# Performance work log

Measured on AMD Instinct MI355X. Metric: run time of the kernel, lower is better.

## Reference

```python
import jax, jax.numpy as jnp
import numpy as np

SEQ = 4096
INPUT_DIM = 64
D_MODEL = 1024
LAYERS = 2


def setup_inputs() -> dict:
    key = jax.random.key(0)
    ks = jax.random.split(key, 7)
    s = 1.0 / np.sqrt(D_MODEL)  # torch-style uniform-ish scale, keeps gates unsaturated
    return {
        "input_market_values": jax.random.normal(ks[0], (SEQ, INPUT_DIM), jnp.float32),
        "W1": jax.random.normal(ks[1], (D_MODEL, INPUT_DIM), jnp.float32) / np.sqrt(INPUT_DIM),
        "b1": jax.random.normal(ks[2], (D_MODEL,), jnp.float32) * s,
        "Wih": jax.random.normal(ks[3], (LAYERS, 4 * D_MODEL, D_MODEL), jnp.float32) * s,
        "Whh": jax.random.normal(ks[4], (LAYERS, 4 * D_MODEL, D_MODEL), jnp.float32) * s,
        "bih": jax.random.normal(ks[5], (LAYERS, 4 * D_MODEL), jnp.float32) * s,
        "bhh": jax.random.normal(ks[6], (LAYERS, 4 * D_MODEL), jnp.float32) * s,
    }


def _lstm_layer(x, Wih, Whh, bih, bhh):
    # x: (T, H_in). PyTorch LSTM gate order: i, f, g, o.
    H = Whh.shape[1]
    b = bih + bhh
    xg = x @ Wih.T + b  # precompute input contribution for all timesteps: (T, 4H)

    def step(carry, xgt):
        h, c = carry
        g = xgt + h @ Whh.T
        i, f, gg, o = jnp.split(g, 4, axis=-1)
        c = jax.nn.sigmoid(f) * c + jax.nn.sigmoid(i) * jnp.tanh(gg)
        h = jax.nn.sigmoid(o) * jnp.tanh(c)
        return (h, c), h

    init = (jnp.zeros((H,), x.dtype), jnp.zeros((H,), x.dtype))
    _, hs = jax.lax.scan(step, init, xg)
    return hs  # (T, H)


def reference(input_market_values, W1, b1, Wih, Whh, bih, bhh):
    # Per-step Linear + LeakyReLU (equivalent to applying it to the whole sequence)
    x = jax.nn.leaky_relu(input_market_values @ W1.T + b1)  # (T, D)
    for l in range(Wih.shape[0]):  # small fixed number of layers
        x = _lstm_layer(x, Wih[l], Whh[l], bih[l], bhh[l])
    # Original returns leaky_relu of the top-layer output at the final timestep, shape (1,1,D)
    return jax.nn.leaky_relu(x[-1]).reshape(1, 1, -1)
```

## Files before the change

### kernel.cpp

```cpp
#include <hip/hip_runtime.h>
#include <hip/hip_fp16.h>
#include <math.h>

#define T_SEQ 4096
#define DIN   64
#define DM    1024
#define G4    4096
#define LSTRIDE_W ((size_t)G4 * DM)
#define LSTRIDE_B ((size_t)G4)

#define SENT 0x7FC0DEADu

#define S_RING  32
#define S_RETRY 4
#define S_HIST  8

typedef unsigned long long u64;
typedef unsigned int u32;

#define PAUSE(n) do { __builtin_amdgcn_s_sleep(n); asm volatile("" ::: "memory"); } while (0)

__device__ __forceinline__ float sigmoidf_(float x) {
    return 1.0f / (1.0f + __expf(-x));
}
__device__ __forceinline__ float tanhf_(float x) {
    float ax = fabsf(x);
    float e  = __expf(-2.0f * ax);
    float t  = (1.0f - e) / (1.0f + e);
    return copysignf(t, x);
}
__device__ __forceinline__ float lrelu_(float x) {
    return x > 0.0f ? x : 0.01f * x;
}

__device__ __forceinline__ u32 pk2_(float x, float y) {
    typedef __fp16 hv2 __attribute__((ext_vector_type(2)));
    union { hv2 h; u32 u; } c;
    c.h = __builtin_amdgcn_cvt_pkrtz(x, y);
    return c.u;
}
#if __has_builtin(__builtin_amdgcn_fdot2)
__device__ __forceinline__ float d2a_(u32 a, u32 b, float acc) {
    typedef __fp16 hv2 __attribute__((ext_vector_type(2)));
    union { u32 u; hv2 h; } ua, ub;
    ua.u = a; ub.u = b;
    return __builtin_amdgcn_fdot2(ua.h, ub.h, acc, false);
}
#else
__device__ __forceinline__ float d2a_(u32 a, u32 b, float acc) {
    union { u32 u; __half2 h; } ua, ub;
    ua.u = a; ub.u = b;
    float2 fa = __half22float2(ua.h);
    float2 fb = __half22float2(ub.h);
    return acc + fa.x * fb.x + fa.y * fb.y;
}
#endif
__device__ __forceinline__ float dot8a_(uint4 q, uint4 h, float acc) {
    acc = d2a_(q.x, h.x, acc);
    acc = d2a_(q.y, h.y, acc);
    acc = d2a_(q.z, h.z, acc);
    acc = d2a_(q.w, h.w, acc);
    return acc;
}

__global__ __launch_bounds__(256) void k_input(const float* __restrict__ inp,
                                               const float* __restrict__ W1,
                                               const float* __restrict__ b1,
                                               float* __restrict__ x) {
    __shared__ float s_in[DIN];
    const int t   = blockIdx.x;
    const int tid = threadIdx.x;
    if (tid < DIN) s_in[tid] = inp[(size_t)t * DIN + tid];
    __syncthreads();
#pragma unroll
    for (int q = 0; q < 4; q++) {
        const int d = tid + q * 256;
        const float4* wr = (const float4*)(W1 + (size_t)d * DIN);
        float acc = 0.0f;
#pragma unroll
        for (int e = 0; e < 16; e++) {
            float4 w = wr[e];
            acc += w.x * s_in[e * 4 + 0] + w.y * s_in[e * 4 + 1] +
                   w.z * s_in[e * 4 + 2] + w.w * s_in[e * 4 + 3];
        }
        acc += b1[d];
        x[(size_t)t * DM + d] = lrelu_(acc);
    }
}

__global__ __launch_bounds__(256) void k_gemm(const float* __restrict__ A,
                                              const float* __restrict__ B,
                                              const float* __restrict__ bih,
                                              const float* __restrict__ bhh,
                                              float* __restrict__ C) {
    const int K = DM;
    __shared__ float As[16][132];
    __shared__ float Bs[16][132];
    const int tid = threadIdx.x;
    const int m0 = blockIdx.y * 128, n0 = blockIdx.x * 128;
    const int tx = tid & 15, ty = tid >> 4;
    const int lr = tid >> 1;
    const int lc = (tid & 1) * 8;

    float acc[8][8] = {};
    const float4* ag = (const float4*)(A + (size_t)(m0 + lr) * K + lc);
    const float4* bg = (const float4*)(B + (size_t)(n0 + lr) * K + lc);

    for (int k0 = 0; k0 < K; k0 += 16) {
        float4 a0 = ag[0], a1 = ag[1];
        float4 b0 = bg[0], b1v = bg[1];
        ag += 4; bg += 4;
        __syncthreads();
        As[lc + 0][lr] = a0.x; As[lc + 1][lr] = a0.y; As[lc + 2][lr] = a0.z; As[lc + 3][lr] = a0.w;
        As[lc + 4][lr] = a1.x; As[lc + 5][lr] = a1.y; As[lc + 6][lr] = a1.z; As[lc + 7][lr] = a1.w;
        Bs[lc + 0][lr] = b0.x; Bs[lc + 1][lr] = b0.y; Bs[lc + 2][lr] = b0.z; Bs[lc + 3][lr] = b0.w;
        Bs[lc + 4][lr] = b1v.x; Bs[lc + 5][lr] = b1v.y; Bs[lc + 6][lr] = b1v.z; Bs[lc + 7][lr] = b1v.w;
        __syncthreads();
#pragma unroll
        for (int k = 0; k < 16; k++) {
            float a[8], b[8];
            *(float4*)&a[0] = *(const float4*)&As[k][ty * 8 + 0];
            *(float4*)&a[4] = *(const float4*)&As[k][ty * 8 + 4];
            *(float4*)&b[0] = *(const float4*)&Bs[k][tx * 8 + 0];
            *(float4*)&b[4] = *(const float4*)&Bs[k][tx * 8 + 4];
#pragma unroll
            for (int i = 0; i < 8; i++)
#pragma unroll
                for (int j = 0; j < 8; j++)
                    acc[i][j] += a[i] * b[j];
        }
    }
    float bj[8];
#pragma unroll
    for (int j = 0; j < 8; j++) {
        int n = n0 + tx * 8 + j;
        bj[j] = bih[n] + bhh[n];
    }
#pragma unroll
    for (int i = 0; i < 8; i++) {
        float4 v0, v1;
        v0.x = acc[i][0] + bj[0]; v0.y = acc[i][1] + bj[1];
        v0.z = acc[i][2] + bj[2]; v0.w = acc[i][3] + bj[3];
        v1.x = acc[i][4] + bj[4]; v1.y = acc[i][5] + bj[5];
        v1.z = acc[i][6] + bj[6]; v1.w = acc[i][7] + bj[7];
        float* cp = C + (size_t)(m0 + ty * 8 + i) * G4 + n0 + tx * 8;
        *(float4*)(cp + 0) = v0;
        *(float4*)(cp + 4) = v1;
    }
}

__global__ __launch_bounds__(256) void k_clear(u32* __restrict__ p) {
    uint4 v; v.x = SENT; v.y = SENT; v.z = SENT; v.w = SENT;
    ((uint4*)p)[(size_t)blockIdx.x * 256 + threadIdx.x] = v;
}

__global__ __launch_bounds__(256, 2) void k_scan2(
        const float* __restrict__ xg,
        const float* __restrict__ Wih1,
        const float* __restrict__ Whh0,
        const float* __restrict__ Whh1,
        const float* __restrict__ bih1,
        const float* __restrict__ bhh1,
        u32* h0hist,
        u64* sl1,
        float* __restrict__ out) {
    const int tid  = threadIdx.x;
    const bool isL0 = (blockIdx.x < 256);
    const int w    = isL0 ? blockIdx.x : (blockIdx.x - 256);
    const int wv   = tid >> 6;
    const int ln   = tid & 63;
    const int rs   = tid >> 4;
    const int ck   = tid & 15;
    const int g_i  = rs & 3;
    const int r    = g_i * DM + w * 4 + wv;

    __shared__ uint4 hstA[2][16][9];
    __shared__ uint4 hstB[2][16][9];

    const int stc = tid >> 4;
    const int sto = tid & 15;

    if (isL0) {
        uint4 wr0[8];
        {
            const float4* gw = (const float4*)(Whh0 + (size_t)r * DM + ck * 64);
#pragma unroll
            for (int e = 0; e < 8; e++) {
                float4 a = gw[2 * e], b = gw[2 * e + 1];
                uint4 q;
                q.x = pk2_(a.x, a.y); q.y = pk2_(a.z, a.w);
                q.z = pk2_(b.x, b.y); q.w = pk2_(b.z, b.w);
                wr0[e] = q;
            }
        }
        float c0 = 0.f, h0v = 0.f;
        float xgv = (ck == 0) ? xg[r] : 0.f;

        for (int t = 0; t < T_SEQ; t++) {
            const int par = t & 1;
            if (t == 0) {
                ((u64*)&hstA[0][stc][0])[sto] = 0ull;
            } else {
                PAUSE(S_RING);
                const u32* hp = h0hist + (size_t)(t - 1) * DM + tid * 4;
                u32 v0, v1, v2, v3;
                for (;;) {
                    v0 = __hip_atomic_load(hp + 0, __ATOMIC_RELAXED, __HIP_MEMORY_SCOPE_AGENT);
                    v1 = __hip_atomic_load(hp + 1, __ATOMIC_RELAXED, __HIP_MEMORY_SCOPE_AGENT);
                    v2 = __hip_atomic_load(hp + 2, __ATOMIC_RELAXED, __HIP_MEMORY_SCOPE_AGENT);
                    v3 = __hip_atomic_load(hp + 3, __ATOMIC_RELAXED, __HIP_MEMORY_SCOPE_AGENT);
                    if ((v0 != SENT) & (v1 != SENT) & (v2 != SENT) & (v3 != SENT)) break;
                    PAUSE(S_RETRY);
                }
                u32 q0 = pk2_(__uint_as_float(v0), __uint_as_float(v1));
                u32 q1 = pk2_(__uint_as_float(v2), __uint_as_float(v3));
                ((u64*)&hstA[par][stc][0])[sto] = ((u64)q1 << 32) | q0;
            }
            __syncthreads();

            float acc = 0.f;
#pragma unroll
            for (int e = 0; e < 8; e++)
                acc = dot8a_(wr0[e], hstA[par][ck][e], acc);
#pragma unroll
            for (int m = 1; m <= 8; m <<= 1) acc += __shfl_xor(acc, m, 64);
            if (ck == 0) acc += xgv;

            float pi = __shfl(acc, 0, 64);
            float pf = __shfl(acc, 16, 64);
            float pg = __shfl(acc, 32, 64);
            float po = __shfl(acc, 48, 64);
            if (ln == 0) {
                c0 = sigmoidf_(pf) * c0 + sigmoidf_(pi) * tanhf_(pg);
                h0v = sigmoidf_(po) * tanhf_(c0);
                __hip_atomic_store(h0hist + (size_t)t * DM + w * 4 + wv,
                                   __float_as_uint(h0v),
                                   __ATOMIC_RELAXED, __HIP_MEMORY_SCOPE_AGENT);
            }
            float xgn = 0.f;
            if (ck == 0 && t + 1 < T_SEQ) xgn = xg[(size_t)(t + 1) * G4 + r];
            xgv = xgn;
        }
    } else {
        uint4 wi1[8], wh1[8];
        {
            const float4* ga = (const float4*)(Wih1 + (size_t)r * DM + ck * 64);
            const float4* gb = (const float4*)(Whh1 + (size_t)r * DM + ck * 64);
#pragma unroll
            for (int e = 0; e < 8; e++) {
                float4 a = ga[2 * e], b = ga[2 * e + 1];
                uint4 q;
                q.x = pk2_(a.x, a.y); q.y = pk2_(a.z, a.w);
                q.z = pk2_(b.x, b.y); q.w = pk2_(b.z, b.w);
                wi1[e] = q;
                a = gb[2 * e]; b = gb[2 * e + 1];
                q.x = pk2_(a.x, a.y); q.y = pk2_(a.z, a.w);
                q.z = pk2_(b.x, b.y); q.w = pk2_(b.z, b.w);
                wh1[e] = q;
            }
        }
        float b1s[4] = {0.f, 0.f, 0.f, 0.f};
        if (ln == 0) {
#pragma unroll
            for (int gg = 0; gg < 4; gg++)
                b1s[gg] = bih1[gg * DM + w * 4 + wv] + bhh1[gg * DM + w * 4 + wv];
        }
        float c1 = 0.f, h1v = 0.f;

        for (int t = 0; t < T_SEQ; t++) {
            const int par = t & 1;
            const u32* hp = h0hist + (size_t)t * DM + tid * 4;

            u32 v0 = __hip_atomic_load(hp + 0, __ATOMIC_RELAXED, __HIP_MEMORY_SCOPE_AGENT);
            u32 v1 = __hip_atomic_load(hp + 1, __ATOMIC_RELAXED, __HIP_MEMORY_SCOPE_AGENT);
            u32 v2 = __hip_atomic_load(hp + 2, __ATOMIC_RELAXED, __HIP_MEMORY_SCOPE_AGENT);
            u32 v3 = __hip_atomic_load(hp + 3, __ATOMIC_RELAXED, __HIP_MEMORY_SCOPE_AGENT);

            if (t > 0) PAUSE(S_RING);

            while ((v0 == SENT) | (v1 == SENT) | (v2 == SENT) | (v3 == SENT)) {
                PAUSE(S_HIST);
                v0 = __hip_atomic_load(hp + 0, __ATOMIC_RELAXED, __HIP_MEMORY_SCOPE_AGENT);
                v1 = __hip_atomic_load(hp + 1, __ATOMIC_RELAXED, __HIP_MEMORY_SCOPE_AGENT);
                v2 = __hip_atomic_load(hp + 2, __ATOMIC_RELAXED, __HIP_MEMORY_SCOPE_AGENT);
                v3 = __hip_atomic_load(hp + 3, __ATOMIC_RELAXED, __HIP_MEMORY_SCOPE_AGENT);
            }
            {
                u32 q0 = pk2_(__uint_as_float(v0), __uint_as_float(v1));
                u32 q1 = pk2_(__uint_as_float(v2), __uint_as_float(v3));
                ((u64*)&hstA[par][stc][0])[sto] = ((u64)q1 << 32) | q0;
            }

            if (t == 0) {
                ((u64*)&hstB[0][stc][0])[sto] = 0ull;
            } else {
                const u64* p1 = sl1 + (size_t)par * 1024 + tid * 4;
                const u32 want = (u32)t;
                u64 d0, d1, d2, d3;
                for (;;) {
                    d0 = __hip_atomic_load(p1 + 0, __ATOMIC_RELAXED, __HIP_MEMORY_SCOPE_AGENT);
                    d1 = __hip_atomic_load(p1 + 1, __ATOMIC_RELAXED, __HIP_MEMORY_SCOPE_AGENT);
                    d2 = __hip_atomic_load(p1 + 2, __ATOMIC_RELAXED, __HIP_MEMORY_SCOPE_AGENT);
                    d3 = __hip_atomic_load(p1 + 3, __ATOMIC_RELAXED, __HIP_MEMORY_SCOPE_AGENT);
                    bool ok = ((u32)(d0 >> 32) == want) & ((u32)(d1 >> 32) == want) &
                              ((u32)(d2 >> 32) == want) & ((u32)(d3 >> 32) == want);
                    if (ok) break;
                    PAUSE(S_RETRY);
                }
                u32 q0 = pk2_(__uint_as_float((u32)d0), __uint_as_float((u32)d1));
                u32 q1 = pk2_(__uint_as_float((u32)d2), __uint_as_float((u32)d3));
                ((u64*)&hstB[par][stc][0])[sto] = ((u64)q1 << 32) | q0;
            }
            __syncthreads();

            float a1 = 0.f, a2 = 0.f;
#pragma unroll
            for (int e = 0; e < 8; e++) {
                a1 = dot8a_(wi1[e], hstA[par][ck][e], a1);
                a2 = dot8a_(wh1[e], hstB[par][ck][e], a2);
            }
#pragma unroll
            for (int m = 1; m <= 8; m <<= 1) {
                a1 += __shfl_xor(a1, m, 64);
                a2 += __shfl_xor(a2, m, 64);
            }
            float pi = __shfl(a1, 0, 64)  + __shfl(a2, 0, 64);
            float pf = __shfl(a1, 16, 64) + __shfl(a2, 16, 64);
            float pg = __shfl(a1, 32, 64) + __shfl(a2, 32, 64);
            float po = __shfl(a1, 48, 64) + __shfl(a2, 48, 64);
            if (ln == 0) {
                pi += b1s[0]; pf += b1s[1]; pg += b1s[2]; po += b1s[3];
                c1 = sigmoidf_(pf) * c1 + sigmoidf_(pi) * tanhf_(pg);
                h1v = sigmoidf_(po) * tanhf_(c1);
                u64 v = ((u64)(u32)(t + 1) << 32) | (u64)__float_as_uint(h1v);
                __hip_atomic_store(sl1 + (size_t)((t + 1) & 1) * 1024 + w * 4 + wv,
                                   v, __ATOMIC_RELAXED, __HIP_MEMORY_SCOPE_AGENT);
            }
        }
        if (ln == 0) out[w * 4 + wv] = lrelu_(h1v);
    }
}

extern "C" void kernel_launch(void* const* d_in, const int* in_sizes, int n_in,
                              void* d_out, int out_size, void* d_ws, size_t ws_size,
                              hipStream_t stream) {
    const float* inp = (const float*)d_in[0];
    const float* W1  = (const float*)d_in[1];
    const float* b1  = (const float*)d_in[2];
    const float* Wih = (const float*)d_in[3];
    const float* Whh = (const float*)d_in[4];
    const float* bih = (const float*)d_in[5];
    const float* bhh = (const float*)d_in[6];
    float* out = (float*)d_out;

    float* x   = (float*)d_ws;
    float* xg  = x + (size_t)T_SEQ * DM;
    u64*   sl1 = (u64*)(xg + (size_t)T_SEQ * G4);
    u32*   h0hist = (u32*)x;
    (void)in_sizes; (void)n_in; (void)out_size; (void)ws_size;

    k_input<<<dim3(T_SEQ), dim3(256), 0, stream>>>(inp, W1, b1, x);

    k_gemm<<<dim3(32, 32), dim3(256), 0, stream>>>(x, Wih, bih, bhh, xg);

    k_clear<<<dim3(4096), dim3(256), 0, stream>>>(h0hist);

    k_scan2<<<dim3(512), dim3(256), 0, stream>>>(
        xg, Wih + LSTRIDE_W, Whh, Whh + LSTRIDE_W,
        bih + LSTRIDE_B, bhh + LSTRIDE_B, h0hist, sl1, out);
}
```

Before: 10.13 ms.

## Publish hidden states as fp16 history with sentinel polling and parallel gate activations

Both LSTM layers now publish each hidden value as a single fp16 halfword into per-timestep history buffers checked against a 16-bit sentinel. Consumers poll with one 64-bit atomic load per thread instead of four 32-bit loads, and the data goes straight to shared memory without repacking. Layer 1 uses a history buffer instead of the two-slot tagged ring and overlaps the input-side dot product with waiting for its own previous state. Gate nonlinearities are computed in parallel across lanes before the shuffle, and the sleep constants are retuned. The risk is that an fp16 result equal to the sentinel pattern (a NaN encoding) would make a consumer spin forever.

```diff
diff --git a/kernel.cpp b/kernel.cpp
--- a/kernel.cpp
+++ b/kernel.cpp
@@ -9,14 +9,16 @@
 #define LSTRIDE_W ((size_t)G4 * DM)
 #define LSTRIDE_B ((size_t)G4)
 
-#define SENT 0x7FC0DEADu
-
-#define S_RING  32
-#define S_RETRY 4
+#define SENT16 0xDEADu
+#define SENT32 0xDEADDEADu
+
+#define S_RING  40
+#define S_RETRY 6
 #define S_HIST  8
 
 typedef unsigned long long u64;
 typedef unsigned int u32;
+typedef unsigned short u16;
 
 #define PAUSE(n) do { __builtin_amdgcn_s_sleep(n); asm volatile("" ::: "memory"); } while (0)
 
@@ -61,6 +63,10 @@
     acc = d2a_(q.z, h.z, acc);
     acc = d2a_(q.w, h.w, acc);
     return acc;
+}
+__device__ __forceinline__ bool has_sent_(u64 v) {
+    return (((u32)v & 0xFFFFu) == SENT16) | ((((u32)v >> 16)) == SENT16) |
+           (((u32)(v >> 32) & 0xFFFFu) == SENT16) | (((u32)(v >> 48)) == SENT16);
 }
 
 __global__ __launch_bounds__(256) void k_input(const float* __restrict__ inp,
@@ -150,7 +156,7 @@
 }
 
 __global__ __launch_bounds__(256) void k_clear(u32* __restrict__ p) {
-    uint4 v; v.x = SENT; v.y = SENT; v.z = SENT; v.w = SENT;
+    uint4 v; v.x = SENT32; v.y = SENT32; v.z = SENT32; v.w = SENT32;
     ((uint4*)p)[(size_t)blockIdx.x * 256 + threadIdx.x] = v;
 }
 
@@ -161,8 +167,8 @@
         const float* __restrict__ Whh1,
         const float* __restrict__ bih1,
         const float* __restrict__ bhh1,
-        u32* h0hist,
-        u64* sl1,
+        u16* h0h,
+        u16* h1h,
         float* __restrict__ out) {
     const int tid  = threadIdx.x;
     const bool isL0 = (blockIdx.x < 256);
@@ -202,19 +208,14 @@
                 ((u64*)&hstA[0][stc][0])[sto] = 0ull;
             } else {
                 PAUSE(S_RING);
-                const u32* hp = h0hist + (size_t)(t - 1) * DM + tid * 4;
-                u32 v0, v1, v2, v3;
+                const u64* hp = (const u64*)(h0h + (size_t)(t - 1) * DM) + tid;
+                u64 v;
                 for (;;) {
-                    v0 = __hip_atomic_load(hp + 0, __ATOMIC_RELAXED, __HIP_MEMORY_SCOPE_AGENT);
-                    v1 = __hip_atomic_load(hp + 1, __ATOMIC_RELAXED, __HIP_MEMORY_SCOPE_AGENT);
-                    v2 = __hip_atomic_load(hp + 2, __ATOMIC_RELAXED, __HIP_MEMORY_SCOPE_AGENT);
-                    v3 = __hip_atomic_load(hp + 3, __ATOMIC_RELAXED, __HIP_MEMORY_SCOPE_AGENT);
-                    if ((v0 != SENT) & (v1 != SENT) & (v2 != SENT) & (v3 != SENT)) break;
+                    v = __hip_atomic_load(hp, __ATOMIC_RELAXED, __HIP_MEMORY_SCOPE_AGENT);
+                    if (!has_sent_(v)) break;
                     PAUSE(S_RETRY);
                 }
-                u32 q0 = pk2_(__uint_as_float(v0), __uint_as_float(v1));
-                u32 q1 = pk2_(__uint_as_float(v2), __uint_as_float(v3));
-                ((u64*)&hstA[par][stc][0])[sto] = ((u64)q1 << 32) | q0;
+                ((u64*)&hstA[par][stc][0])[sto] = v;
             }
             __syncthreads();
 
@@ -226,15 +227,16 @@
             for (int m = 1; m <= 8; m <<= 1) acc += __shfl_xor(acc, m, 64);
             if (ck == 0) acc += xgv;
 
-            float pi = __shfl(acc, 0, 64);
-            float pf = __shfl(acc, 16, 64);
-            float pg = __shfl(acc, 32, 64);
-            float po = __shfl(acc, 48, 64);
+            float act = ((ln >> 4) == 2) ? tanhf_(acc) : sigmoidf_(acc);
+            float ai = __shfl(act, 0, 64);
+            float af = __shfl(act, 16, 64);
+            float ag = __shfl(act, 32, 64);
+            float ao = __shfl(act, 48, 64);
             if (ln == 0) {
-                c0 = sigmoidf_(pf) * c0 + sigmoidf_(pi) * tanhf_(pg);
-                h0v = sigmoidf_(po) * tanhf_(c0);
-                __hip_atomic_store(h0hist + (size_t)t * DM + w * 4 + wv,
-                                   __float_as_uint(h0v),
+                c0  = af * c0 + ai * ag;
+                h0v = ao * tanhf_(c0);
+                u32 q = pk2_(h0v, h0v);
+                __hip_atomic_store(h0h + (size_t)t * DM + w * 4 + wv, (u16)(q & 0xFFFFu),
                                    __ATOMIC_RELAXED, __HIP_MEMORY_SCOPE_AGENT);
             }
             float xgn = 0.f;
@@ -259,82 +261,70 @@
                 wh1[e] = q;
             }
         }
-        float b1s[4] = {0.f, 0.f, 0.f, 0.f};
-        if (ln == 0) {
-#pragma unroll
-            for (int gg = 0; gg < 4; gg++)
-                b1s[gg] = bih1[gg * DM + w * 4 + wv] + bhh1[gg * DM + w * 4 + wv];
+        float bsel = 0.f;
+        if ((ln & 15) == 0) {
+            const int gg = ln >> 4;
+            bsel = bih1[gg * DM + w * 4 + wv] + bhh1[gg * DM + w * 4 + wv];
         }
         float c1 = 0.f, h1v = 0.f;
 
         for (int t = 0; t < T_SEQ; t++) {
             const int par = t & 1;
-            const u32* hp = h0hist + (size_t)t * DM + tid * 4;
-
-            u32 v0 = __hip_atomic_load(hp + 0, __ATOMIC_RELAXED, __HIP_MEMORY_SCOPE_AGENT);
-            u32 v1 = __hip_atomic_load(hp + 1, __ATOMIC_RELAXED, __HIP_MEMORY_SCOPE_AGENT);
-            u32 v2 = __hip_atomic_load(hp + 2, __ATOMIC_RELAXED, __HIP_MEMORY_SCOPE_AGENT);
-            u32 v3 = __hip_atomic_load(hp + 3, __ATOMIC_RELAXED, __HIP_MEMORY_SCOPE_AGENT);
+            const u64* hp0 = (const u64*)(h0h + (size_t)t * DM) + tid;
+            const u64* hp1 = (const u64*)(h1h + (size_t)(t > 0 ? t - 1 : 0) * DM) + tid;
+
+            u64 v0 = __hip_atomic_load(hp0, __ATOMIC_RELAXED, __HIP_MEMORY_SCOPE_AGENT);
 
             if (t > 0) PAUSE(S_RING);
 
-            while ((v0 == SENT) | (v1 == SENT) | (v2 == SENT) | (v3 == SENT)) {
+            while (has_sent_(v0)) {
                 PAUSE(S_HIST);
-                v0 = __hip_atomic_load(hp + 0, __ATOMIC_RELAXED, __HIP_MEMORY_SCOPE_AGENT);
-                v1 = __hip_atomic_load(hp + 1, __ATOMIC_RELAXED, __HIP_MEMORY_SCOPE_AGENT);
-                v2 = __hip_atomic_load(hp + 2, __ATOMIC_RELAXED, __HIP_MEMORY_SCOPE_AGENT);
-                v3 = __hip_atomic_load(hp + 3, __ATOMIC_RELAXED, __HIP_MEMORY_SCOPE_AGENT);
-            }
-            {
-                u32 q0 = pk2_(__uint_as_float(v0), __uint_as_float(v1));
-                u32 q1 = pk2_(__uint_as_float(v2), __uint_as_float(v3));
-                ((u64*)&hstA[par][stc][0])[sto] = ((u64)q1 << 32) | q0;
-            }
+                v0 = __hip_atomic_load(hp0, __ATOMIC_RELAXED, __HIP_MEMORY_SCOPE_AGENT);
+            }
+            ((u64*)&hstA[par][stc][0])[sto] = v0;
+
+            u64 v1 = 0;
+            if (t > 0)
+                v1 = __hip_atomic_load(hp1, __ATOMIC_RELAXED, __HIP_MEMORY_SCOPE_AGENT);
+            __syncthreads();
+
+            float a1 = 0.f;
+#pragma unroll
+            for (int e = 0; e < 8; e++)
+                a1 = dot8a_(wi1[e], hstA[par][ck][e], a1);
+#pragma unroll
+            for (int m = 1; m <= 8; m <<= 1) a1 += __shfl_xor(a1, m, 64);
 
             if (t == 0) {
                 ((u64*)&hstB[0][stc][0])[sto] = 0ull;
             } else {
-                const u64* p1 = sl1 + (size_t)par * 1024 + tid * 4;
-                const u32 want = (u32)t;
-                u64 d0, d1, d2, d3;
-                for (;;) {
-                    d0 = __hip_atomic_load(p1 + 0, __ATOMIC_RELAXED, __HIP_MEMORY_SCOPE_AGENT);
-                    d1 = __hip_atomic_load(p1 + 1, __ATOMIC_RELAXED, __HIP_MEMORY_SCOPE_AGENT);
-                    d2 = __hip_atomic_load(p1 + 2, __ATOMIC_RELAXED, __HIP_MEMORY_SCOPE_AGENT);
-                    d3 = __hip_atomic_load(p1 + 3, __ATOMIC_RELAXED, __HIP_MEMORY_SCOPE_AGENT);
-                    bool ok = ((u32)(d0 >> 32) == want) & ((u32)(d1 >> 32) == want) &
-                              ((u32)(d2 >> 32) == want) & ((u32)(d3 >> 32) == want);
-                    if (ok) break;
+                while (has_sent_(v1)) {
                     PAUSE(S_RETRY);
+                    v1 = __hip_atomic_load(hp1, __ATOMIC_RELAXED, __HIP_MEMORY_SCOPE_AGENT);
                 }
-                u32 q0 = pk2_(__uint_as_float((u32)d0), __uint_as_float((u32)d1));
-                u32 q1 = pk2_(__uint_as_float((u32)d2), __uint_as_float((u32)d3));
-                ((u64*)&hstB[par][stc][0])[sto] = ((u64)q1 << 32) | q0;
+                ((u64*)&hstB[par][stc][0])[sto] = v1;
             }
             __syncthreads();
 
-            float a1 = 0.f, a2 = 0.f;
-#pragma unroll
-            for (int e = 0; e < 8; e++) {
-                a1 = dot8a_(wi1[e], hstA[par][ck][e], a1);
+            float a2 = 0.f;
+#pragma unroll
+            for (int e = 0; e < 8; e++)
                 a2 = dot8a_(wh1[e], hstB[par][ck][e], a2);
-            }
-#pragma unroll
-            for (int m = 1; m <= 8; m <<= 1) {
-                a1 += __shfl_xor(a1, m, 64);
-                a2 += __shfl_xor(a2, m, 64);
-            }
-            float pi = __shfl(a1, 0, 64)  + __shfl(a2, 0, 64);
-            float pf = __shfl(a1, 16, 64) + __shfl(a2, 16, 64);
-            float pg = __shfl(a1, 32, 64) + __shfl(a2, 32, 64);
-            float po = __shfl(a1, 48, 64) + __shfl(a2, 48, 64);
+#pragma unroll
+            for (int m = 1; m <= 8; m <<= 1) a2 += __shfl_xor(a2, m, 64);
+
+            float p = (a1 + a2) + bsel;
+            float act = ((ln >> 4) == 2) ? tanhf_(p) : sigmoidf_(p);
+            float ai = __shfl(act, 0, 64);
+            float af = __shfl(act, 16, 64);
+            float ag = __shfl(act, 32, 64);
+            float ao = __shfl(act, 48, 64);
             if (ln == 0) {
-                pi += b1s[0]; pf += b1s[1]; pg += b1s[2]; po += b1s[3];
-                c1 = sigmoidf_(pf) * c1 + sigmoidf_(pi) * tanhf_(pg);
-                h1v = sigmoidf_(po) * tanhf_(c1);
-                u64 v = ((u64)(u32)(t + 1) << 32) | (u64)__float_as_uint(h1v);
-                __hip_atomic_store(sl1 + (size_t)((t + 1) & 1) * 1024 + w * 4 + wv,
-                                   v, __ATOMIC_RELAXED, __HIP_MEMORY_SCOPE_AGENT);
+                c1  = af * c1 + ai * ag;
+                h1v = ao * tanhf_(c1);
+                u32 q = pk2_(h1v, h1v);
+                __hip_atomic_store(h1h + (size_t)t * DM + w * 4 + wv, (u16)(q & 0xFFFFu),
+                                   __ATOMIC_RELAXED, __HIP_MEMORY_SCOPE_AGENT);
             }
         }
         if (ln == 0) out[w * 4 + wv] = lrelu_(h1v);
@@ -355,17 +345,17 @@
 
     float* x   = (float*)d_ws;
     float* xg  = x + (size_t)T_SEQ * DM;
-    u64*   sl1 = (u64*)(xg + (size_t)T_SEQ * G4);
-    u32*   h0hist = (u32*)x;
+    u16*   h0h = (u16*)d_ws;
+    u16*   h1h = (u16*)d_ws + (size_t)T_SEQ * DM;
     (void)in_sizes; (void)n_in; (void)out_size; (void)ws_size;
 
     k_input<<<dim3(T_SEQ), dim3(256), 0, stream>>>(inp, W1, b1, x);
 
     k_gemm<<<dim3(32, 32), dim3(256), 0, stream>>>(x, Wih, bih, bhh, xg);
 
-    k_clear<<<dim3(4096), dim3(256), 0, stream>>>(h0hist);
+    k_clear<<<dim3(4096), dim3(256), 0, stream>>>((u32*)d_ws);
 
     k_scan2<<<dim3(512), dim3(256), 0, stream>>>(
         xg, Wih + LSTRIDE_W, Whh, Whh + LSTRIDE_W,
-        bih + LSTRIDE_B, bhh + LSTRIDE_B, h0hist, sl1, out);
-}
+        bih + LSTRIDE_B, bhh + LSTRIDE_B, h0h, h1h, out);
+}
```

New measurement: 13.36 ms. 1.32x slower.
